# Kernel tuning notes

Hardware: AMD Instinct MI355X
Metric: run time of the kernel (lower is better)

## Reference

```python
import jax, jax.numpy as jnp
import numpy as np

EMBED_DIM = 512
NUM_JOINTS = 17
HIDDEN = EMBED_DIM * 2  # hidden_ratio=2
B, T = 32, 243


def setup_inputs() -> dict:
    key = jax.random.key(0)
    k_x, k_w1, k_w2 = jax.random.split(key, 3)
    x = jax.random.normal(k_x, (B, T, NUM_JOINTS, EMBED_DIM), dtype=jnp.float32)
    # kaiming_uniform with a=sqrt(5): bound = sqrt(6 / ((1 + a^2) * fan_in)) = sqrt(1/fan_in)
    b1 = float(np.sqrt(1.0 / EMBED_DIM))
    fc1_w = jax.random.uniform(k_w1, (NUM_JOINTS, EMBED_DIM, HIDDEN), minval=-b1, maxval=b1, dtype=jnp.float32)
    fc1_b = jnp.zeros((NUM_JOINTS, HIDDEN), dtype=jnp.float32)
    b2 = float(np.sqrt(1.0 / HIDDEN))
    fc2_w = jax.random.uniform(k_w2, (NUM_JOINTS, HIDDEN, 3), minval=-b2, maxval=b2, dtype=jnp.float32)
    fc2_b = jnp.zeros((NUM_JOINTS, 3), dtype=jnp.float32)
    ln_gamma = jnp.ones((EMBED_DIM,), dtype=jnp.float32)
    ln_beta = jnp.zeros((EMBED_DIM,), dtype=jnp.float32)
    return {"x": x, "ln_gamma": ln_gamma, "ln_beta": ln_beta,
            "fc1_w": fc1_w, "fc1_b": fc1_b, "fc2_w": fc2_w, "fc2_b": fc2_b}


def _layernorm(x, gamma, beta, eps=1e-5):
    mu = jnp.mean(x, axis=-1, keepdims=True)
    var = jnp.mean(jnp.square(x - mu), axis=-1, keepdims=True)
    return (x - mu) * jax.lax.rsqrt(var + eps) * gamma + beta


def reference(x, ln_gamma, ln_beta, fc1_w, fc1_b, fc2_w, fc2_b):
    # x: [B, T, J, d] -> [B, T, J, 3]
    xn = _layernorm(x, ln_gamma, ln_beta)
    h = jnp.einsum('btjd,jdh->btjh', xn, fc1_w) + fc1_b  # [B,T,J,H]
    h = jax.nn.gelu(h, approximate=False)  # torch GELU default is exact (erf)
    y = jnp.einsum('btjh,jho->btjo', h, fc2_w) + fc2_b  # [B,T,J,3]
    return y
```

## Files before the change

kernel.cpp:

```cpp
#include <hip/hip_runtime.h>
#include <hip/hip_bf16.h>

#define JN   17
#define DIM  512
#define HID  1024
#define MTOT 7776
#define MPAD 7808
#define NTHR 512

typedef __attribute__((ext_vector_type(8))) short s16x8;
typedef __attribute__((ext_vector_type(4))) float f32x4;
typedef unsigned short ushort_t;

__device__ __forceinline__ unsigned int f2bf(float f) {
    return (unsigned int)__builtin_bit_cast(unsigned short, __float2bfloat16(f));
}

__device__ __forceinline__ float gelu_erf(float h) {
    float ah = fabsf(h);
    float z  = ah * 0.7071067811865476f;
    float t  = __builtin_amdgcn_rcpf(fmaf(0.3275911f, z, 1.0f));
    float p  = fmaf(fmaf(fmaf(fmaf(1.061405429f, t, -1.453152027f), t,
                              1.421413741f), t, -0.284496736f), t, 0.254829592f);
    float er = 1.0f - p * t * __expf(-z * z);
    return fmaf(0.5f * ah, er, 0.5f * h);
}

__global__ __launch_bounds__(256)
void prep_w1(const float* __restrict__ w1, ushort_t* __restrict__ w1s) {
    int b  = blockIdx.x;
    int nq = b & 3;
    int kc = (b >> 2) & 15;
    int j  = b >> 6;
    int n  = nq * 256 + threadIdx.x;

    const float* src = w1 + ((size_t)j * DIM + kc * 32) * HID + n;
    ushort_t* dst = w1s + (((size_t)j * 16 + kc) * 1024 + n) * 32;

    #pragma unroll
    for (int u = 0; u < 4; ++u) {
        float v[8];
        #pragma unroll
        for (int e = 0; e < 8; ++e) v[e] = src[(u * 8 + e) * HID];
        uint4 qq;
        qq.x = f2bf(v[0]) | (f2bf(v[1]) << 16);
        qq.y = f2bf(v[2]) | (f2bf(v[3]) << 16);
        qq.z = f2bf(v[4]) | (f2bf(v[5]) << 16);
        qq.w = f2bf(v[6]) | (f2bf(v[7]) << 16);
        int p = u ^ ((n >> 1) & 3);
        *(uint4*)(dst + p * 8) = qq;
    }
}

__global__ __launch_bounds__(NTHR)
void prep_xn(const float* __restrict__ x,
             const float* __restrict__ gamma,
             const float* __restrict__ beta,
             ushort_t* __restrict__ xa)
{
    const int lane = threadIdx.x & 63;
    const int wv   = threadIdx.x >> 6;
    const int m    = blockIdx.x * 8 + wv;
    const int j    = blockIdx.y;

    const float4* gp = (const float4*)(gamma + lane * 8);
    const float4* bp = (const float4*)(beta + lane * 8);
    float4 g0 = gp[0], g1 = gp[1];
    float4 e0 = bp[0], e1 = bp[1];

    const float4* xp = (const float4*)(x + ((size_t)m * JN + j) * DIM + lane * 8);
    float4 va = xp[0], vb = xp[1];

    float s  = ((va.x + va.y) + (va.z + va.w)) + ((vb.x + vb.y) + (vb.z + vb.w));
    float s2 = fmaf(va.x, va.x, fmaf(va.y, va.y, fmaf(va.z, va.z, fmaf(va.w, va.w,
               fmaf(vb.x, vb.x, fmaf(vb.y, vb.y, fmaf(vb.z, vb.z, vb.w * vb.w)))))));
    #pragma unroll
    for (int d = 1; d < 64; d <<= 1) {
        s  += __shfl_xor(s,  d);
        s2 += __shfl_xor(s2, d);
    }
    float mu  = s * (1.0f / 512.0f);
    float var = s2 * (1.0f / 512.0f) - mu * mu;
    float rs  = rsqrtf(var + 1e-5f);

    float v0 = fmaf((va.x - mu) * rs, g0.x, e0.x);
    float v1 = fmaf((va.y - mu) * rs, g0.y, e0.y);
    float v2 = fmaf((va.z - mu) * rs, g0.z, e0.z);
    float v3 = fmaf((va.w - mu) * rs, g0.w, e0.w);
    float v4 = fmaf((vb.x - mu) * rs, g1.x, e1.x);
    float v5 = fmaf((vb.y - mu) * rs, g1.y, e1.y);
    float v6 = fmaf((vb.z - mu) * rs, g1.z, e1.z);
    float v7 = fmaf((vb.w - mu) * rs, g1.w, e1.w);
    uint4 qq;
    qq.x = f2bf(v0) | (f2bf(v1) << 16);
    qq.y = f2bf(v2) | (f2bf(v3) << 16);
    qq.z = f2bf(v4) | (f2bf(v5) << 16);
    qq.w = f2bf(v6) | (f2bf(v7) << 16);

    int kc = lane >> 2;
    *(uint4*)(xa + (((size_t)j * 16 + kc) * MPAD + m) * 32 + (lane & 3) * 8) = qq;
}

#define NWG10 (122 * 4 * JN)

__global__ __launch_bounds__(256, 3)
void pjh_gemm_v10(const ushort_t* __restrict__ xa,
                  const ushort_t* __restrict__ w1s,
                  const float* __restrict__ b1,
                  const float* __restrict__ w2,
                  float* __restrict__ ypart)
{
    __shared__ float Yp[4 * 64 * 3];
    const int tid  = threadIdx.x;
    const int lane = tid & 63;
    const int wn   = tid >> 6;

    const int xcd  = blockIdx.x & 7;
    const int lid  = blockIdx.x >> 3;
    const int work = xcd * (NWG10 / 8) + lid;
    const int nt3  = work & 3;
    const int wrest = work >> 2;
    const int mt   = wrest % 122;
    const int j    = wrest / 122;

    const int g = lane >> 4;
    const ushort_t* aB = xa + (size_t)j * 16 * MPAD * 32
                            + ((size_t)mt * 64 + (lane & 15)) * 32 + g * 8;
    const int pB = g ^ (((lane & 15) >> 1) & 3);
    const ushort_t* bB = w1s + (size_t)j * 16 * 1024 * 32
                             + ((size_t)nt3 * 256 + wn * 64 + (lane & 15)) * 32 + pB * 8;

#define LOADSET(FA, FB) do {                                                   \
        _Pragma("unroll")                                                      \
        for (int mf = 0; mf < 4; ++mf) FA[mf] = *(const s16x8*)(aB + mf * 512);\
        _Pragma("unroll")                                                      \
        for (int nf = 0; nf < 4; ++nf) FB[nf] = *(const s16x8*)(bB + nf * 512);\
        aB += (size_t)MPAD * 32;                                               \
        bB += 32768;                                                           \
    } while (0)

#define COMPUTE(FA, FB) do {                                                   \
        __builtin_amdgcn_s_setprio(1);                                         \
        _Pragma("unroll")                                                      \
        for (int mf = 0; mf < 4; ++mf)                                         \
            _Pragma("unroll")                                                  \
            for (int nf = 0; nf < 4; ++nf)                                     \
                acc[mf][nf] = __builtin_amdgcn_mfma_f32_16x16x32_bf16(FA[mf], FB[nf], acc[mf][nf], 0, 0, 0); \
        __builtin_amdgcn_s_setprio(0);                                         \
    } while (0)

    const f32x4 zero4 = {0.f, 0.f, 0.f, 0.f};
    f32x4 acc[4][4];
    #pragma unroll
    for (int mf = 0; mf < 4; ++mf)
        #pragma unroll
        for (int nf = 0; nf < 4; ++nf) acc[mf][nf] = zero4;

    s16x8 fA0[4], fB0[4], fA1[4], fB1[4];

    LOADSET(fA0, fB0);
    LOADSET(fA1, fB1);
    #pragma unroll 1
    for (int tp = 0; tp < 7; ++tp) {
        COMPUTE(fA0, fB0);
        LOADSET(fA0, fB0);
        COMPUTE(fA1, fB1);
        LOADSET(fA1, fB1);
    }
    COMPUTE(fA0, fB0);
    COMPUTE(fA1, fB1);

    float yr[4][4][3];
    #pragma unroll
    for (int a = 0; a < 4; ++a)
        #pragma unroll
        for (int rr = 0; rr < 4; ++rr)
            #pragma unroll
            for (int o = 0; o < 3; ++o) yr[a][rr][o] = 0.f;

    #pragma unroll
    for (int nf = 0; nf < 4; ++nf) {
        int n = nt3 * 256 + wn * 64 + nf * 16 + (lane & 15);
        float b1v = b1[j * HID + n];
        const float* w2p = w2 + ((size_t)j * HID + n) * 3;
        float w20 = w2p[0], w21 = w2p[1], w22 = w2p[2];
        #pragma unroll
        for (int mf = 0; mf < 4; ++mf) {
            #pragma unroll
            for (int rr = 0; rr < 4; ++rr) {
                float gv = gelu_erf(acc[mf][nf][rr] + b1v);
                yr[mf][rr][0] = fmaf(gv, w20, yr[mf][rr][0]);
                yr[mf][rr][1] = fmaf(gv, w21, yr[mf][rr][1]);
                yr[mf][rr][2] = fmaf(gv, w22, yr[mf][rr][2]);
            }
        }
    }

    #pragma unroll
    for (int mf = 0; mf < 4; ++mf)
        #pragma unroll
        for (int rr = 0; rr < 4; ++rr)
            #pragma unroll
            for (int o = 0; o < 3; ++o) {
                float v = yr[mf][rr][o];
                v += __shfl_xor(v, 1);
                v += __shfl_xor(v, 2);
                v += __shfl_xor(v, 4);
                v += __shfl_xor(v, 8);
                yr[mf][rr][o] = v;
            }

    if ((lane & 15) == 0) {
        int mrow = lane >> 4;
        #pragma unroll
        for (int mf = 0; mf < 4; ++mf)
            #pragma unroll
            for (int rr = 0; rr < 4; ++rr) {
                int m = mf * 16 + mrow * 4 + rr;
                #pragma unroll
                for (int o = 0; o < 3; ++o)
                    Yp[(wn * 64 + m) * 3 + o] = yr[mf][rr][o];
            }
    }
    __syncthreads();

    for (int idx = tid; idx < 64 * 3; idx += 256) {
        int m = idx / 3;
        int o = idx - m * 3;
        int gr = mt * 64 + m;
        if (gr < MTOT) {
            float v = Yp[m * 3 + o] + Yp[(64 + m) * 3 + o]
                    + Yp[(128 + m) * 3 + o] + Yp[(192 + m) * 3 + o];
            ypart[(((size_t)nt3 * MPAD + gr) * JN + j) * 3 + o] = v;
        }
    }
#undef LOADSET
#undef COMPUTE
}

__global__ __launch_bounds__(512)
void fc2_reduce(const float* __restrict__ ypart,
                const float* __restrict__ b2,
                float* __restrict__ out)
{
    int idx = blockIdx.x * 512 + threadIdx.x;
    if (idx >= MTOT * JN * 3) return;
    int rest = idx / 3;
    int o = idx - rest * 3;
    int j = rest % JN;
    const size_t sl = (size_t)MPAD * JN * 3;
    float v = b2[j * 3 + o];
    #pragma unroll
    for (int s = 0; s < 4; ++s) v += ypart[s * sl + idx];
    out[idx] = v;
}

#define BM3 96
#define A3_OFF 0
#define B3_OFF 98304
#define Y3_OFF 98304
#define SMEM_V3 163840

__global__ __launch_bounds__(NTHR, 2)
void pjh_fused_v3(const float* __restrict__ x,
                  const float* __restrict__ gamma,
                  const float* __restrict__ beta,
                  const ushort_t* __restrict__ w1s,
                  const float* __restrict__ b1,
                  const float* __restrict__ w2,
                  const float* __restrict__ b2,
                  float* __restrict__ out)
{
    extern __shared__ char smem[];
    const int tid  = threadIdx.x;
    const int lane = tid & 63;
    const int wv   = tid >> 6;
    const int wm   = wv >> 2;
    const int wn   = wv & 3;
    const int mt   = blockIdx.x;
    const int j    = blockIdx.y;

    const ushort_t* w1j = w1s + (size_t)j * 16 * 1024 * 32;

    #pragma unroll
    for (int tt = 0; tt < 2; ++tt) {
        const ushort_t* tb = w1j + (size_t)tt * 1024 * 32;
        #pragma unroll
        for (int qq = 0; qq < 2; ++qq) {
            const ushort_t* src = tb + (size_t)(wv * 2 + qq) * 512 + lane * 8;
            void* dst = smem + B3_OFF + tt * 16384 + (wv * 2 + qq) * 1024;
            __builtin_amdgcn_global_load_lds(
                (const __attribute__((address_space(1))) unsigned int*)src,
                (__attribute__((address_space(3))) unsigned int*)dst, 16, 0, 0);
        }
    }

    {
        const float4* gp  = (const float4*)(gamma + lane * 8);
        const float4* bpp = (const float4*)(beta + lane * 8);
        float4 g0 = gp[0], g1 = gp[1];
        float4 e0 = bpp[0], e1 = bpp[1];
        #pragma unroll
        for (int rb = 0; rb < 12; rb += 4) {
            float4 xs[4][2];
            #pragma unroll
            for (int rr = 0; rr < 4; ++rr) {
                int gr = mt * BM3 + wv * 12 + rb + rr;
                const float4* xp = (const float4*)(x + ((size_t)gr * JN + j) * DIM + lane * 8);
                xs[rr][0] = xp[0]; xs[rr][1] = xp[1];
            }
            #pragma unroll
            for (int rr = 0; rr < 4; ++rr) {
                int m = wv * 12 + rb + rr;
                float4 va = xs[rr][0], vb = xs[rr][1];
                float s  = ((va.x + va.y) + (va.z + va.w)) + ((vb.x + vb.y) + (vb.z + vb.w));
                float s2 = fmaf(va.x, va.x, fmaf(va.y, va.y, fmaf(va.z, va.z, fmaf(va.w, va.w,
                           fmaf(vb.x, vb.x, fmaf(vb.y, vb.y, fmaf(vb.z, vb.z, vb.w * vb.w)))))));
                #pragma unroll
                for (int d = 1; d < 64; d <<= 1) {
                    s  += __shfl_xor(s,  d);
                    s2 += __shfl_xor(s2, d);
                }
                float mu  = s * (1.0f / 512.0f);
                float var = s2 * (1.0f / 512.0f) - mu * mu;
                float rs  = rsqrtf(var + 1e-5f);
                float v0 = fmaf((va.x - mu) * rs, g0.x, e0.x);
                float v1 = fmaf((va.y - mu) * rs, g0.y, e0.y);
                float v2 = fmaf((va.z - mu) * rs, g0.z, e0.z);
                float v3 = fmaf((va.w - mu) * rs, g0.w, e0.w);
                float v4 = fmaf((vb.x - mu) * rs, g1.x, e1.x);
                float v5 = fmaf((vb.y - mu) * rs, g1.y, e1.y);
                float v6 = fmaf((vb.z - mu) * rs, g1.z, e1.z);
                float v7 = fmaf((vb.w - mu) * rs, g1.w, e1.w);
                uint4 qq;
                qq.x = f2bf(v0) | (f2bf(v1) << 16);
                qq.y = f2bf(v2) | (f2bf(v3) << 16);
                qq.z = f2bf(v4) | (f2bf(v5) << 16);
                qq.w = f2bf(v6) | (f2bf(v7) << 16);
                *(uint4*)(smem + A3_OFF + m * 1024 + ((lane ^ (m & 7)) * 16)) = qq;
            }
        }
    }

    __syncthreads();

    float yr[3][4][3];
    #pragma unroll
    for (int a = 0; a < 3; ++a)
        #pragma unroll
        for (int rr = 0; rr < 4; ++rr)
            #pragma unroll
            for (int o = 0; o < 3; ++o) yr[a][rr][o] = 0.f;

    const f32x4 zero4 = {0.f, 0.f, 0.f, 0.f};
    f32x4 acc[3][4];
    #pragma unroll
    for (int mf = 0; mf < 3; ++mf)
        #pragma unroll
        for (int nf = 0; nf < 4; ++nf) acc[mf][nf] = zero4;

    #pragma unroll 1
    for (int t = 0; t < 64; ++t) {
        if (t + 2 < 64) {
            int kc = (t + 2) & 15, nt = (t + 2) >> 4;
            const ushort_t* tb = w1j + ((size_t)kc * 1024 + nt * 256) * 32;
            int bb = ((t + 2) & 3) * 16384;
            #pragma unroll
            for (int qq = 0; qq < 2; ++qq) {
                const ushort_t* src = tb + (size_t)(wv * 2 + qq) * 512 + lane * 8;
                void* dst = smem + B3_OFF + bb + (wv * 2 + qq) * 1024;
                __builtin_amdgcn_global_load_lds(
                    (const __attribute__((address_space(1))) unsigned int*)src,
                    (__attribute__((address_space(3))) unsigned int*)dst, 16, 0, 0);
            }
        }

        int kc = t & 15;
        int bb = (t & 3) * 16384;
        int g  = lane >> 4;
        s16x8 aF[3], bF[4];
        #pragma unroll
        for (int mf = 0; mf < 3; ++mf) {
            int m  = wm * 48 + mf * 16 + (lane & 15);
            int ul = kc * 4 + g;
            aF[mf] = *(const s16x8*)(smem + A3_OFF + m * 1024 + ((ul ^ (m & 7)) * 16));
        }
        #pragma unroll
        for (int nf = 0; nf < 4; ++nf) {
            int nl = wn * 64 + nf * 16 + (lane & 15);
            int p  = g ^ ((nl >> 1) & 3);
            bF[nf] = *(const s16x8*)(smem + B3_OFF + bb + (nl * 4 + p) * 16);
        }

        __builtin_amdgcn_s_setprio(1);
        #pragma unroll
        for (int mf = 0; mf < 3; ++mf)
            #pragma unroll
            for (int nf = 0; nf < 4; ++nf)
                acc[mf][nf] = __builtin_amdgcn_mfma_f32_16x16x32_bf16(aF[mf], bF[nf], acc[mf][nf], 0, 0, 0);
        __builtin_amdgcn_s_setprio(0);

        if ((t & 15) == 15) {
            int nt = t >> 4;
            #pragma unroll
            for (int nf = 0; nf < 4; ++nf) {
                int n = nt * 256 + wn * 64 + nf * 16 + (lane & 15);
                float b1v = b1[j * HID + n];
                const float* w2p = w2 + ((size_t)j * HID + n) * 3;
                float w20 = w2p[0], w21 = w2p[1], w22 = w2p[2];
                #pragma unroll
                for (int mf = 0; mf < 3; ++mf) {
                    #pragma unroll
                    for (int rr = 0; rr < 4; ++rr) {
                        float gv = gelu_erf(acc[mf][nf][rr] + b1v);
                        yr[mf][rr][0] = fmaf(gv, w20, yr[mf][rr][0]);
                        yr[mf][rr][1] = fmaf(gv, w21, yr[mf][rr][1]);
                        yr[mf][rr][2] = fmaf(gv, w22, yr[mf][rr][2]);
                    }
                }
            }
            #pragma unroll
            for (int mf = 0; mf < 3; ++mf)
                #pragma unroll
                for (int nf = 0; nf < 4; ++nf)
                    acc[mf][nf] = zero4;
        }

        if (t < 62) {
            asm volatile("s_waitcnt vmcnt(2)" ::: "memory");
        } else {
            asm volatile("s_waitcnt vmcnt(0)" ::: "memory");
        }
        __builtin_amdgcn_s_barrier();
    }

    #pragma unroll
    for (int mf = 0; mf < 3; ++mf)
        #pragma unroll
        for (int rr = 0; rr < 4; ++rr)
            #pragma unroll
            for (int o = 0; o < 3; ++o) {
                float v = yr[mf][rr][o];
                v += __shfl_xor(v, 1);
                v += __shfl_xor(v, 2);
                v += __shfl_xor(v, 4);
                v += __shfl_xor(v, 8);
                yr[mf][rr][o] = v;
            }

    __syncthreads();

    float* Yp = (float*)(smem + Y3_OFF);
    if ((lane & 15) == 0) {
        int mrow = lane >> 4;
        #pragma unroll
        for (int mf = 0; mf < 3; ++mf)
            #pragma unroll
            for (int rr = 0; rr < 4; ++rr) {
                int m = wm * 48 + mf * 16 + mrow * 4 + rr;
                #pragma unroll
                for (int o = 0; o < 3; ++o)
                    Yp[(wn * BM3 + m) * 3 + o] = yr[mf][rr][o];
            }
    }
    __syncthreads();

    if (tid < BM3 * 3) {
        int m = tid / 3;
        int o = tid - m * 3;
        int gr = mt * BM3 + m;
        float v = Yp[m * 3 + o] + Yp[(BM3 + m) * 3 + o]
                + Yp[(2 * BM3 + m) * 3 + o] + Yp[(3 * BM3 + m) * 3 + o]
                + b2[j * 3 + o];
        out[((size_t)gr * JN + j) * 3 + o] = v;
    }
}

extern "C" void kernel_launch(void* const* d_in, const int* in_sizes, int n_in,
                              void* d_out, int out_size, void* d_ws, size_t ws_size,
                              hipStream_t stream) {
    (void)in_sizes; (void)n_in; (void)out_size;
    const float* x   = (const float*)d_in[0];
    const float* ga  = (const float*)d_in[1];
    const float* be  = (const float*)d_in[2];
    const float* w1  = (const float*)d_in[3];
    const float* b1  = (const float*)d_in[4];
    const float* w2  = (const float*)d_in[5];
    const float* b2  = (const float*)d_in[6];
    float* out = (float*)d_out;

    const size_t xa_bytes  = (size_t)JN * 16 * MPAD * 32 * sizeof(ushort_t);
    const size_t w1s_bytes = (size_t)JN * 16 * 1024 * 32 * sizeof(ushort_t);
    const size_t yp_bytes  = (size_t)4 * MPAD * JN * 3 * sizeof(float);

    if (ws_size >= xa_bytes + w1s_bytes + yp_bytes) {
        ushort_t* xa  = (ushort_t*)d_ws;
        ushort_t* w1s = (ushort_t*)((char*)d_ws + xa_bytes);
        float* ypart  = (float*)((char*)d_ws + xa_bytes + w1s_bytes);
        prep_xn<<<dim3(MTOT / 8, JN), NTHR, 0, stream>>>(x, ga, be, xa);
        prep_w1<<<JN * 16 * 4, 256, 0, stream>>>(w1, w1s);
        pjh_gemm_v10<<<NWG10, 256, 0, stream>>>(xa, w1s, b1, w2, ypart);
        fc2_reduce<<<(MTOT * JN * 3 + 511) / 512, 512, 0, stream>>>(ypart, b2, out);
    } else {
        ushort_t* w1s = (ushort_t*)d_ws;
        prep_w1<<<JN * 16 * 4, 256, 0, stream>>>(w1, w1s);
        hipFuncSetAttribute((const void*)pjh_fused_v3,
                            hipFuncAttributeMaxDynamicSharedMemorySize, SMEM_V3);
        dim3 grid(MTOT / BM3, JN);
        pjh_fused_v3<<<grid, NTHR, SMEM_V3, stream>>>(x, ga, be, w1s, b1, w2, b2, out);
    }
}
```

Before: 319.1 us.

## Make GEMM workgroups persistent over four M-tiles and hoist epilogue weight loads

Each workgroup now handles four consecutive 64-row M tiles for one joint and N quarter instead of one, cutting the grid from 8296 to 2108 workgroups. MPAD grows to a multiple of 256 to fit the larger groups. Bias and fc2 weights are loaded once and the epilogue is restructured to reduce per row, with the pipeline prefetching the next tile's fragments before the epilogue runs. The XCD work mapping now handles a grid size that is not a multiple of 8. Fewer workgroups mean less launch and epilogue-setup overhead, but the grid of 2108 may leave CUs underused and cause tail imbalance. The W1 fragments are reloaded for every tile rather than reused.

```diff
diff --git a/kernel.cpp b/kernel.cpp
--- a/kernel.cpp
+++ b/kernel.cpp
@@ -5,7 +5,7 @@
 #define DIM  512
 #define HID  1024
 #define MTOT 7776
-#define MPAD 7808
+#define MPAD 7936
 #define NTHR 512
 
 typedef __attribute__((ext_vector_type(8))) short s16x8;
@@ -101,10 +101,10 @@
     *(uint4*)(xa + (((size_t)j * 16 + kc) * MPAD + m) * 32 + (lane & 3) * 8) = qq;
 }
 
-#define NWG10 (122 * 4 * JN)
+#define NWG11 (31 * 4 * JN)
 
 __global__ __launch_bounds__(256, 3)
-void pjh_gemm_v10(const ushort_t* __restrict__ xa,
+void pjh_gemm_v11(const ushort_t* __restrict__ xa,
                   const ushort_t* __restrict__ w1s,
                   const float* __restrict__ b1,
                   const float* __restrict__ w2,
@@ -115,20 +115,33 @@
     const int lane = tid & 63;
     const int wn   = tid >> 6;
 
-    const int xcd  = blockIdx.x & 7;
-    const int lid  = blockIdx.x >> 3;
-    const int work = xcd * (NWG10 / 8) + lid;
+    const int q   = NWG11 / 8, r = NWG11 % 8;
+    const int xcd = blockIdx.x & 7;
+    const int lid = blockIdx.x >> 3;
+    const int work = ((xcd < r) ? xcd * (q + 1) : r * (q + 1) + (xcd - r) * q) + lid;
     const int nt3  = work & 3;
-    const int wrest = work >> 2;
-    const int mt   = wrest % 122;
-    const int j    = wrest / 122;
-
-    const int g = lane >> 4;
-    const ushort_t* aB = xa + (size_t)j * 16 * MPAD * 32
-                            + ((size_t)mt * 64 + (lane & 15)) * 32 + g * 8;
-    const int pB = g ^ (((lane & 15) >> 1) & 3);
-    const ushort_t* bB = w1s + (size_t)j * 16 * 1024 * 32
-                             + ((size_t)nt3 * 256 + wn * 64 + (lane & 15)) * 32 + pB * 8;
+    const int rest = work >> 2;
+    const int mtg  = rest % 31;
+    const int j    = rest / 31;
+
+    const int kg = lane >> 4;
+    const ushort_t* aB0 = xa + (size_t)j * 16 * MPAD * 32
+                             + ((size_t)mtg * 256 + (lane & 15)) * 32 + kg * 8;
+    const int pB = kg ^ (((lane & 15) >> 1) & 3);
+    const ushort_t* bB0 = w1s + (size_t)j * 16 * 1024 * 32
+                              + ((size_t)nt3 * 256 + wn * 64 + (lane & 15)) * 32 + pB * 8;
+
+    float b1v[4], w20[4], w21[4], w22[4];
+    #pragma unroll
+    for (int nf = 0; nf < 4; ++nf) {
+        int n = nt3 * 256 + wn * 64 + nf * 16 + (lane & 15);
+        b1v[nf] = b1[j * HID + n];
+        const float* w2p = w2 + ((size_t)j * HID + n) * 3;
+        w20[nf] = w2p[0]; w21[nf] = w2p[1]; w22[nf] = w2p[2];
+    }
+
+    const ushort_t* aB = aB0;
+    const ushort_t* bB = bB0;
 
 #define LOADSET(FA, FB) do {                                                   \
         _Pragma("unroll")                                                      \
@@ -160,79 +173,68 @@
 
     LOADSET(fA0, fB0);
     LOADSET(fA1, fB1);
+
     #pragma unroll 1
-    for (int tp = 0; tp < 7; ++tp) {
+    for (int gg = 0; gg < 4; ++gg) {
+        #pragma unroll 1
+        for (int tp = 0; tp < 7; ++tp) {
+            COMPUTE(fA0, fB0); LOADSET(fA0, fB0);
+            COMPUTE(fA1, fB1); LOADSET(fA1, fB1);
+        }
         COMPUTE(fA0, fB0);
-        LOADSET(fA0, fB0);
+        if (gg < 3) {
+            aB = aB0 + (size_t)(gg + 1) * 2048;
+            bB = bB0;
+            LOADSET(fA0, fB0);
+        }
         COMPUTE(fA1, fB1);
-        LOADSET(fA1, fB1);
-    }
-    COMPUTE(fA0, fB0);
-    COMPUTE(fA1, fB1);
-
-    float yr[4][4][3];
-    #pragma unroll
-    for (int a = 0; a < 4; ++a)
-        #pragma unroll
-        for (int rr = 0; rr < 4; ++rr)
-            #pragma unroll
-            for (int o = 0; o < 3; ++o) yr[a][rr][o] = 0.f;
-
-    #pragma unroll
-    for (int nf = 0; nf < 4; ++nf) {
-        int n = nt3 * 256 + wn * 64 + nf * 16 + (lane & 15);
-        float b1v = b1[j * HID + n];
-        const float* w2p = w2 + ((size_t)j * HID + n) * 3;
-        float w20 = w2p[0], w21 = w2p[1], w22 = w2p[2];
+        if (gg < 3) {
+            LOADSET(fA1, fB1);
+        }
+
         #pragma unroll
         for (int mf = 0; mf < 4; ++mf) {
             #pragma unroll
             for (int rr = 0; rr < 4; ++rr) {
-                float gv = gelu_erf(acc[mf][nf][rr] + b1v);
-                yr[mf][rr][0] = fmaf(gv, w20, yr[mf][rr][0]);
-                yr[mf][rr][1] = fmaf(gv, w21, yr[mf][rr][1]);
-                yr[mf][rr][2] = fmaf(gv, w22, yr[mf][rr][2]);
-            }
-        }
-    }
-
-    #pragma unroll
-    for (int mf = 0; mf < 4; ++mf)
-        #pragma unroll
-        for (int rr = 0; rr < 4; ++rr)
-            #pragma unroll
-            for (int o = 0; o < 3; ++o) {
-                float v = yr[mf][rr][o];
-                v += __shfl_xor(v, 1);
-                v += __shfl_xor(v, 2);
-                v += __shfl_xor(v, 4);
-                v += __shfl_xor(v, 8);
-                yr[mf][rr][o] = v;
-            }
-
-    if ((lane & 15) == 0) {
-        int mrow = lane >> 4;
+                float s0 = 0.f, s1 = 0.f, s2 = 0.f;
+                #pragma unroll
+                for (int nf = 0; nf < 4; ++nf) {
+                    float gv = gelu_erf(acc[mf][nf][rr] + b1v[nf]);
+                    s0 = fmaf(gv, w20[nf], s0);
+                    s1 = fmaf(gv, w21[nf], s1);
+                    s2 = fmaf(gv, w22[nf], s2);
+                }
+                s0 += __shfl_xor(s0, 1); s0 += __shfl_xor(s0, 2);
+                s0 += __shfl_xor(s0, 4); s0 += __shfl_xor(s0, 8);
+                s1 += __shfl_xor(s1, 1); s1 += __shfl_xor(s1, 2);
+                s1 += __shfl_xor(s1, 4); s1 += __shfl_xor(s1, 8);
+                s2 += __shfl_xor(s2, 1); s2 += __shfl_xor(s2, 2);
+                s2 += __shfl_xor(s2, 4); s2 += __shfl_xor(s2, 8);
+                if ((lane & 15) == 0) {
+                    int m = mf * 16 + (lane >> 4) * 4 + rr;
+                    Yp[(wn * 64 + m) * 3 + 0] = s0;
+                    Yp[(wn * 64 + m) * 3 + 1] = s1;
+                    Yp[(wn * 64 + m) * 3 + 2] = s2;
+                }
+            }
+        }
         #pragma unroll
         for (int mf = 0; mf < 4; ++mf)
             #pragma unroll
-            for (int rr = 0; rr < 4; ++rr) {
-                int m = mf * 16 + mrow * 4 + rr;
-                #pragma unroll
-                for (int o = 0; o < 3; ++o)
-                    Yp[(wn * 64 + m) * 3 + o] = yr[mf][rr][o];
-            }
-    }
-    __syncthreads();
-
-    for (int idx = tid; idx < 64 * 3; idx += 256) {
-        int m = idx / 3;
-        int o = idx - m * 3;
-        int gr = mt * 64 + m;
-        if (gr < MTOT) {
-            float v = Yp[m * 3 + o] + Yp[(64 + m) * 3 + o]
-                    + Yp[(128 + m) * 3 + o] + Yp[(192 + m) * 3 + o];
-            ypart[(((size_t)nt3 * MPAD + gr) * JN + j) * 3 + o] = v;
-        }
+            for (int nf = 0; nf < 4; ++nf) acc[mf][nf] = zero4;
+
+        __syncthreads();
+        for (int idx = tid; idx < 64 * 3; idx += 256) {
+            int m = idx / 3;
+            int o = idx - m * 3;
+            int gr = mtg * 256 + gg * 64 + m;
+            if (gr < MTOT) {
+                float v = Yp[m * 3 + o] + Yp[(64 + m) * 3 + o]
+                        + Yp[(128 + m) * 3 + o] + Yp[(192 + m) * 3 + o];
+                ypart[(((size_t)nt3 * MPAD + gr) * JN + j) * 3 + o] = v;
+            }
+        }
+        __syncthreads();
     }
 #undef LOADSET
 #undef COMPUTE
@@ -499,7 +501,7 @@
         float* ypart  = (float*)((char*)d_ws + xa_bytes + w1s_bytes);
         prep_xn<<<dim3(MTOT / 8, JN), NTHR, 0, stream>>>(x, ga, be, xa);
         prep_w1<<<JN * 16 * 4, 256, 0, stream>>>(w1, w1s);
-        pjh_gemm_v10<<<NWG10, 256, 0, stream>>>(xa, w1s, b1, w2, ypart);
+        pjh_gemm_v11<<<NWG11, 256, 0, stream>>>(xa, w1s, b1, w2, ypart);
         fc2_reduce<<<(MTOT * JN * 3 + 511) / 512, 512, 0, stream>>>(ypart, b2, out);
     } else {
         ushort_t* w1s = (ushort_t*)d_ws;
```

New measurement: 349.1 us. +9.4%, slower.
